# Performance work log

Hardware: AMD Instinct MI355X
Metric: run time of the kernel (lower is better)

Reference implementation:

```python
import jax, jax.numpy as jnp
import numpy as np

EPS = 1e-7
MAX_NORM = 1.0 - 1e-5  # projection radius of the unit Poincare ball (c=1)


def _artanh(x):
    x = jnp.clip(x, -1.0 + 1e-7, 1.0 - 1e-7)
    return 0.5 * (jnp.log1p(x) - jnp.log1p(-x))


def _proj(x):
    # project back onto the open unit ball for numerical stability
    norm = jnp.maximum(jnp.linalg.norm(x, axis=-1, keepdims=True), EPS)
    return jnp.where(norm > MAX_NORM, x / norm * MAX_NORM, x)


def _mobius_add(x, y):
    # x (+) y on the Poincare ball, c = 1
    x2 = jnp.sum(x * x, axis=-1, keepdims=True)
    y2 = jnp.sum(y * y, axis=-1, keepdims=True)
    xy = jnp.sum(x * y, axis=-1, keepdims=True)
    num = (1.0 + 2.0 * xy + y2) * x + (1.0 - x2) * y
    den = 1.0 + 2.0 * xy + x2 * y2
    return num / jnp.maximum(den, EPS)


def _mobius_matvec(x, W):
    # M (x) x = tanh(||Mx||/||x|| * artanh(||x||)) * Mx/||Mx||
    x_norm = jnp.maximum(jnp.linalg.norm(x, axis=-1, keepdims=True), EPS)  # [N,1]
    mx = x @ W.T                                                           # [N,out]
    mx_norm = jnp.maximum(jnp.linalg.norm(mx, axis=-1, keepdims=True), EPS)
    res = jnp.tanh(mx_norm / x_norm * _artanh(x_norm)) * (mx / mx_norm)
    return _proj(res)


def _parallel_transport0(x, v):
    # transport tangent v from origin to x: (lambda_0 / lambda_x) v = (1 - ||x||^2) v
    x2 = jnp.sum(x * x, axis=-1, keepdims=True)
    return (1.0 - x2) * v


def _expmap(x, v):
    # exp_x(v) = x (+) tanh(lambda_x ||v|| / 2) * v / ||v||
    v_norm = jnp.maximum(jnp.linalg.norm(v, axis=-1, keepdims=True), EPS)
    x2 = jnp.sum(x * x, axis=-1, keepdims=True)
    lam = 2.0 / jnp.maximum(1.0 - x2, EPS)
    second = jnp.tanh(0.5 * lam * v_norm) * (v / v_norm)
    return _proj(_mobius_add(x, second))


def setup_inputs() -> dict:
    key = jax.random.key(0)
    kx, kw, kb = jax.random.split(key, 3)
    N, IN, OUT = 262144, 256, 256
    # points strictly inside the unit ball (norm ~ 0.16)
    x = 0.01 * jax.random.normal(kx, (N, IN), dtype=jnp.float32)
    # kaiming_uniform_(a=sqrt(5)) => U(-1/sqrt(fan_in), 1/sqrt(fan_in))
    bound = 1.0 / np.sqrt(IN)
    W = jax.random.uniform(kw, (OUT, IN), dtype=jnp.float32, minval=-bound, maxval=bound)
    b = jax.random.uniform(kb, (OUT,), dtype=jnp.float32, minval=-0.001, maxval=0.001)
    return {"x": x, "W": W, "b": b}


def reference(x, W, b):
    res = _mobius_matvec(x, W)                 # hyperbolic linear transform
    pt = _parallel_transport0(res, b)          # transport bias from origin to res
    return _expmap(res, pt)                    # exponential map at res
```

## Files before the change

kernel.cpp:

```cpp
#include <hip/hip_runtime.h>

#define EPS 1e-7f
#define MAX_NORM (1.0f - 1e-5f)

typedef __attribute__((ext_vector_type(8))) short bf16x8;
typedef __attribute__((ext_vector_type(4))) short short4v;
typedef __attribute__((ext_vector_type(4))) float f32x4;

__device__ __forceinline__ short f2bf(float f){
  unsigned u = __builtin_bit_cast(unsigned, f);
  u = (u + 0x7fffu + ((u >> 16) & 1u)) >> 16;
  return (short)u;
}
__device__ __forceinline__ float bf2f(short s){
  unsigned u = ((unsigned)(unsigned short)s) << 16;
  return __builtin_bit_cast(float, u);
}

__global__ void setup_s_kernel(const float* __restrict__ b, float* __restrict__ s_buf){
  __shared__ float redv[256];
  int t = threadIdx.x;
  float v = b[t];
  redv[t] = v * v;
  __syncthreads();
  for (int off = 128; off > 0; off >>= 1){
    if (t < off) redv[t] += redv[t + off];
    __syncthreads();
  }
  float bn = sqrtf(redv[0]);
  float th = tanhf(bn);
  s_buf[t] = th * v / fmaxf(bn, EPS);
  if (t == 0) s_buf[256] = th * th;
}

__global__ void conv_w_kernel(const float* __restrict__ W, short* __restrict__ WB){
  int idx = blockIdx.x * 256 + threadIdx.x;
  int n = idx >> 8, k = idx & 255;
  int ks = k >> 5, q = (k >> 3) & 3, j = k & 7;
  int dst = ((((n >> 4) * 8 + ks) * 4 + q) * 16 + (n & 15)) * 8 + j;
  WB[dst] = f2bf(W[idx]);
}

__global__ void hyp_main(const float* __restrict__ x, const short* __restrict__ WB,
                         const float* __restrict__ s_buf, float* __restrict__ out){
  __shared__ __align__(16) short A_lds[64 * 264];
  __shared__ float xpart[256];
  __shared__ float redp[4][64][2];
  __shared__ float pq[64][2];

  const int tid = threadIdx.x;
  const int wave = tid >> 6, lane = tid & 63;
  const int quad = lane >> 4, l15 = lane & 15;
  const int m0 = blockIdx.x * 64;

  const float4* xt = (const float4*)(x + (size_t)m0 * 256);
  #pragma unroll
  for (int i = 0; i < 16; i++){
    int f = i * 256 + tid;
    int row = f >> 6, c4 = f & 63;
    float4 v = xt[f];
    short4v p;
    p.x = f2bf(v.x); p.y = f2bf(v.y); p.z = f2bf(v.z); p.w = f2bf(v.w);
    *(short4v*)&A_lds[row * 264 + c4 * 4] = p;
  }
  __syncthreads();

  {
    int row = tid >> 2, seg = tid & 3;
    float sum = 0.f;
    #pragma unroll
    for (int i = 0; i < 8; i++){
      bf16x8 v = *(const bf16x8*)&A_lds[row * 264 + seg * 64 + i * 8];
      #pragma unroll
      for (int j = 0; j < 8; j++){ float f = bf2f(v[j]); sum += f * f; }
    }
    xpart[tid] = sum;
  }

  f32x4 acc[4][4];
  #pragma unroll
  for (int mt = 0; mt < 4; mt++)
    #pragma unroll
    for (int tn = 0; tn < 4; tn++) acc[mt][tn] = (f32x4){0.f, 0.f, 0.f, 0.f};

  const bf16x8* WBv = (const bf16x8*)WB;
  #pragma unroll
  for (int ks = 0; ks < 8; ks++){
    bf16x8 bfrag[4], afrag[4];
    #pragma unroll
    for (int tn = 0; tn < 4; tn++) bfrag[tn] = WBv[((wave * 4 + tn) * 8 + ks) * 64 + lane];
    #pragma unroll
    for (int mt = 0; mt < 4; mt++)
      afrag[mt] = *(const bf16x8*)&A_lds[(mt * 16 + l15) * 264 + ks * 32 + quad * 8];
    #pragma unroll
    for (int mt = 0; mt < 4; mt++)
      #pragma unroll
      for (int tn = 0; tn < 4; tn++)
        acc[mt][tn] = __builtin_amdgcn_mfma_f32_16x16x32_bf16(afrag[mt], bfrag[tn], acc[mt][tn], 0, 0, 0);
  }

  float sv[4];
  #pragma unroll
  for (int tn = 0; tn < 4; tn++) sv[tn] = s_buf[wave * 64 + tn * 16 + l15];

  float msq[4][4], mds[4][4];
  #pragma unroll
  for (int mt = 0; mt < 4; mt++)
    #pragma unroll
    for (int r = 0; r < 4; r++){
      float a = 0.f, d = 0.f;
      #pragma unroll
      for (int tn = 0; tn < 4; tn++){ float c = acc[mt][tn][r]; a += c * c; d += c * sv[tn]; }
      msq[mt][r] = a; mds[mt][r] = d;
    }
  #pragma unroll
  for (int m = 1; m < 16; m <<= 1){
    #pragma unroll
    for (int mt = 0; mt < 4; mt++)
      #pragma unroll
      for (int r = 0; r < 4; r++){
        msq[mt][r] += __shfl_xor(msq[mt][r], m, 64);
        mds[mt][r] += __shfl_xor(mds[mt][r], m, 64);
      }
  }
  if (l15 == 0){
    #pragma unroll
    for (int mt = 0; mt < 4; mt++)
      #pragma unroll
      for (int r = 0; r < 4; r++){
        int row = mt * 16 + quad * 4 + r;
        redp[wave][row][0] = msq[mt][r];
        redp[wave][row][1] = mds[mt][r];
      }
  }
  __syncthreads();

  if (tid < 64){
    int row = tid;
    float ms  = redp[0][row][0] + redp[1][row][0] + redp[2][row][0] + redp[3][row][0];
    float md  = redp[0][row][1] + redp[1][row][1] + redp[2][row][1] + redp[3][row][1];
    float xn2 = xpart[row*4+0] + xpart[row*4+1] + xpart[row*4+2] + xpart[row*4+3];
    float s2 = s_buf[256];
    float xn = fmaxf(sqrtf(xn2), EPS);
    float xc = fminf(xn, 1.0f - 1e-7f);
    float art = 0.5f * (log1pf(xc) - log1pf(-xc));
    float mxn = fmaxf(sqrtf(ms), EPS);
    float tt = tanhf(mxn / xn * art);
    float te = fminf(tt, MAX_NORM);
    float sr = te / mxn;
    float r2 = te * te;
    float xy = sr * md;
    float aa = 1.0f + 2.0f * xy + s2;
    float bc = 1.0f - r2;
    float den = fmaxf(1.0f + 2.0f * xy + r2 * s2, EPS);
    float P = aa * sr / den, Q = bc / den;
    float num2 = aa * aa * r2 + 2.0f * aa * bc * xy + bc * bc * s2;
    float on = fmaxf(sqrtf(num2) / den, EPS);
    if (on > MAX_NORM){ float fsc = MAX_NORM / on; P *= fsc; Q *= fsc; }
    pq[row][0] = P; pq[row][1] = Q;
  }
  __syncthreads();

  float* orow = out + (size_t)m0 * 256;
  #pragma unroll
  for (int mt = 0; mt < 4; mt++)
    #pragma unroll
    for (int r = 0; r < 4; r++){
      int row = mt * 16 + quad * 4 + r;
      float P = pq[row][0], Q = pq[row][1];
      #pragma unroll
      for (int tn = 0; tn < 4; tn++)
        orow[(size_t)row * 256 + wave * 64 + tn * 16 + l15] = P * acc[mt][tn][r] + Q * sv[tn];
    }
}

extern "C" void kernel_launch(void* const* d_in, const int* in_sizes, int n_in,
                              void* d_out, int out_size, void* d_ws, size_t ws_size,
                              hipStream_t stream){
  const float* x = (const float*)d_in[0];
  const float* W = (const float*)d_in[1];
  const float* b = (const float*)d_in[2];
  float* out = (float*)d_out;

  short* WB    = (short*)d_ws;
  float* s_buf = (float*)((char*)d_ws + 256 * 256 * 2);

  int N = in_sizes[0] / 256;

  setup_s_kernel<<<1, 256, 0, stream>>>(b, s_buf);
  conv_w_kernel<<<256, 256, 0, stream>>>(W, WB);
  hyp_main<<<N / 64, 256, 0, stream>>>(x, WB, s_buf, out);
}
```

Before: 478.1 us.

## Compute transposed MFMA per wave on its own rows, dropping LDS and block syncs

Each wave now owns 16 rows and loads x straight from global memory into registers as the MFMA B operand, computing W·x^T so that each lane holds four consecutive output columns of one row. Row norms and the dot product with the bias are reduced with two cross-quad shuffles instead of an LDS staging buffer and two block barriers, and output is written as float4 stores. The x norm is now taken in fp32 before bf16 rounding. In exchange every wave streams the full 256x256 bf16 W from global/L2 rather than a quarter of it, and register pressure rises (16 accumulators plus 8 x fragments), with launch bounds asking for 4 blocks per CU.

```diff
diff --git a/kernel.cpp b/kernel.cpp
--- a/kernel.cpp
+++ b/kernel.cpp
@@ -4,17 +4,12 @@
 #define MAX_NORM (1.0f - 1e-5f)
 
 typedef __attribute__((ext_vector_type(8))) short bf16x8;
-typedef __attribute__((ext_vector_type(4))) short short4v;
 typedef __attribute__((ext_vector_type(4))) float f32x4;
 
 __device__ __forceinline__ short f2bf(float f){
   unsigned u = __builtin_bit_cast(unsigned, f);
   u = (u + 0x7fffu + ((u >> 16) & 1u)) >> 16;
   return (short)u;
-}
-__device__ __forceinline__ float bf2f(short s){
-  unsigned u = ((unsigned)(unsigned short)s) << 16;
-  return __builtin_bit_cast(float, u);
 }
 
 __global__ void setup_s_kernel(const float* __restrict__ b, float* __restrict__ s_buf){
@@ -41,137 +36,95 @@
   WB[dst] = f2bf(W[idx]);
 }
 
-__global__ void hyp_main(const float* __restrict__ x, const short* __restrict__ WB,
-                         const float* __restrict__ s_buf, float* __restrict__ out){
-  __shared__ __align__(16) short A_lds[64 * 264];
-  __shared__ float xpart[256];
-  __shared__ float redp[4][64][2];
-  __shared__ float pq[64][2];
-
+__global__ __launch_bounds__(256, 4)
+void hyp_main(const float* __restrict__ x, const short* __restrict__ WB,
+              const float* __restrict__ s_buf, float* __restrict__ out){
   const int tid = threadIdx.x;
   const int wave = tid >> 6, lane = tid & 63;
   const int quad = lane >> 4, l15 = lane & 15;
-  const int m0 = blockIdx.x * 64;
+  const int row = blockIdx.x * 64 + wave * 16 + l15;
 
-  const float4* xt = (const float4*)(x + (size_t)m0 * 256);
+  const float* xrow = x + (size_t)row * 256;
+  float4 va[8], vb[8];
   #pragma unroll
-  for (int i = 0; i < 16; i++){
-    int f = i * 256 + tid;
-    int row = f >> 6, c4 = f & 63;
-    float4 v = xt[f];
-    short4v p;
-    p.x = f2bf(v.x); p.y = f2bf(v.y); p.z = f2bf(v.z); p.w = f2bf(v.w);
-    *(short4v*)&A_lds[row * 264 + c4 * 4] = p;
-  }
-  __syncthreads();
-
-  {
-    int row = tid >> 2, seg = tid & 3;
-    float sum = 0.f;
-    #pragma unroll
-    for (int i = 0; i < 8; i++){
-      bf16x8 v = *(const bf16x8*)&A_lds[row * 264 + seg * 64 + i * 8];
-      #pragma unroll
-      for (int j = 0; j < 8; j++){ float f = bf2f(v[j]); sum += f * f; }
-    }
-    xpart[tid] = sum;
+  for (int ks = 0; ks < 8; ks++){
+    const float4* p = (const float4*)(xrow + ks * 32 + quad * 8);
+    va[ks] = p[0];
+    vb[ks] = p[1];
   }
 
-  f32x4 acc[4][4];
+  float xn2 = 0.f;
+  bf16x8 xf[8];
   #pragma unroll
-  for (int mt = 0; mt < 4; mt++)
-    #pragma unroll
-    for (int tn = 0; tn < 4; tn++) acc[mt][tn] = (f32x4){0.f, 0.f, 0.f, 0.f};
+  for (int ks = 0; ks < 8; ks++){
+    float f0 = va[ks].x, f1 = va[ks].y, f2 = va[ks].z, f3 = va[ks].w;
+    float f4 = vb[ks].x, f5 = vb[ks].y, f6 = vb[ks].z, f7 = vb[ks].w;
+    xn2 += f0*f0 + f1*f1 + f2*f2 + f3*f3 + f4*f4 + f5*f5 + f6*f6 + f7*f7;
+    bf16x8 p;
+    p[0]=f2bf(f0); p[1]=f2bf(f1); p[2]=f2bf(f2); p[3]=f2bf(f3);
+    p[4]=f2bf(f4); p[5]=f2bf(f5); p[6]=f2bf(f6); p[7]=f2bf(f7);
+    xf[ks] = p;
+  }
+  xn2 += __shfl_xor(xn2, 16, 64);
+  xn2 += __shfl_xor(xn2, 32, 64);
 
   const bf16x8* WBv = (const bf16x8*)WB;
+  f32x4 acc[16];
   #pragma unroll
-  for (int ks = 0; ks < 8; ks++){
-    bf16x8 bfrag[4], afrag[4];
+  for (int tn = 0; tn < 16; tn++){
+    bf16x8 wf[8];
     #pragma unroll
-    for (int tn = 0; tn < 4; tn++) bfrag[tn] = WBv[((wave * 4 + tn) * 8 + ks) * 64 + lane];
+    for (int ks = 0; ks < 8; ks++)
+      wf[ks] = WBv[(tn * 8 + ks) * 64 + lane];
+    f32x4 a = (f32x4){0.f, 0.f, 0.f, 0.f};
     #pragma unroll
-    for (int mt = 0; mt < 4; mt++)
-      afrag[mt] = *(const bf16x8*)&A_lds[(mt * 16 + l15) * 264 + ks * 32 + quad * 8];
-    #pragma unroll
-    for (int mt = 0; mt < 4; mt++)
-      #pragma unroll
-      for (int tn = 0; tn < 4; tn++)
-        acc[mt][tn] = __builtin_amdgcn_mfma_f32_16x16x32_bf16(afrag[mt], bfrag[tn], acc[mt][tn], 0, 0, 0);
+    for (int ks = 0; ks < 8; ks++)
+      a = __builtin_amdgcn_mfma_f32_16x16x32_bf16(wf[ks], xf[ks], a, 0, 0, 0);
+    acc[tn] = a;
   }
 
-  float sv[4];
+  float msq = 0.f, mds = 0.f;
   #pragma unroll
-  for (int tn = 0; tn < 4; tn++) sv[tn] = s_buf[wave * 64 + tn * 16 + l15];
+  for (int tn = 0; tn < 16; tn++){
+    float4 sv4 = *(const float4*)&s_buf[tn * 16 + quad * 4];
+    msq += acc[tn][0]*acc[tn][0] + acc[tn][1]*acc[tn][1]
+         + acc[tn][2]*acc[tn][2] + acc[tn][3]*acc[tn][3];
+    mds += acc[tn][0]*sv4.x + acc[tn][1]*sv4.y + acc[tn][2]*sv4.z + acc[tn][3]*sv4.w;
+  }
+  msq += __shfl_xor(msq, 16, 64);
+  msq += __shfl_xor(msq, 32, 64);
+  mds += __shfl_xor(mds, 16, 64);
+  mds += __shfl_xor(mds, 32, 64);
 
-  float msq[4][4], mds[4][4];
+  float s2 = s_buf[256];
+  float xn = fmaxf(sqrtf(xn2), EPS);
+  float xc = fminf(xn, 1.0f - 1e-7f);
+  float art = 0.5f * (log1pf(xc) - log1pf(-xc));
+  float mxn = fmaxf(sqrtf(msq), EPS);
+  float tt = tanhf(mxn / xn * art);
+  float te = fminf(tt, MAX_NORM);
+  float sr = te / mxn;
+  float r2 = te * te;
+  float xy = sr * mds;
+  float aa = 1.0f + 2.0f * xy + s2;
+  float bc = 1.0f - r2;
+  float den = fmaxf(1.0f + 2.0f * xy + r2 * s2, EPS);
+  float P = aa * sr / den, Q = bc / den;
+  float num2 = aa * aa * r2 + 2.0f * aa * bc * xy + bc * bc * s2;
+  float on = fmaxf(sqrtf(num2) / den, EPS);
+  if (on > MAX_NORM){ float fsc = MAX_NORM / on; P *= fsc; Q *= fsc; }
+
+  float* orow = out + (size_t)row * 256;
   #pragma unroll
-  for (int mt = 0; mt < 4; mt++)
-    #pragma unroll
-    for (int r = 0; r < 4; r++){
-      float a = 0.f, d = 0.f;
-      #pragma unroll
-      for (int tn = 0; tn < 4; tn++){ float c = acc[mt][tn][r]; a += c * c; d += c * sv[tn]; }
-      msq[mt][r] = a; mds[mt][r] = d;
-    }
-  #pragma unroll
-  for (int m = 1; m < 16; m <<= 1){
-    #pragma unroll
-    for (int mt = 0; mt < 4; mt++)
-      #pragma unroll
-      for (int r = 0; r < 4; r++){
-        msq[mt][r] += __shfl_xor(msq[mt][r], m, 64);
-        mds[mt][r] += __shfl_xor(mds[mt][r], m, 64);
-      }
+  for (int tn = 0; tn < 16; tn++){
+    float4 sv4 = *(const float4*)&s_buf[tn * 16 + quad * 4];
+    float4 o;
+    o.x = P * acc[tn][0] + Q * sv4.x;
+    o.y = P * acc[tn][1] + Q * sv4.y;
+    o.z = P * acc[tn][2] + Q * sv4.z;
+    o.w = P * acc[tn][3] + Q * sv4.w;
+    *(float4*)&orow[tn * 16 + quad * 4] = o;
   }
-  if (l15 == 0){
-    #pragma unroll
-    for (int mt = 0; mt < 4; mt++)
-      #pragma unroll
-      for (int r = 0; r < 4; r++){
-        int row = mt * 16 + quad * 4 + r;
-        redp[wave][row][0] = msq[mt][r];
-        redp[wave][row][1] = mds[mt][r];
-      }
-  }
-  __syncthreads();
-
-  if (tid < 64){
-    int row = tid;
-    float ms  = redp[0][row][0] + redp[1][row][0] + redp[2][row][0] + redp[3][row][0];
-    float md  = redp[0][row][1] + redp[1][row][1] + redp[2][row][1] + redp[3][row][1];
-    float xn2 = xpart[row*4+0] + xpart[row*4+1] + xpart[row*4+2] + xpart[row*4+3];
-    float s2 = s_buf[256];
-    float xn = fmaxf(sqrtf(xn2), EPS);
-    float xc = fminf(xn, 1.0f - 1e-7f);
-    float art = 0.5f * (log1pf(xc) - log1pf(-xc));
-    float mxn = fmaxf(sqrtf(ms), EPS);
-    float tt = tanhf(mxn / xn * art);
-    float te = fminf(tt, MAX_NORM);
-    float sr = te / mxn;
-    float r2 = te * te;
-    float xy = sr * md;
-    float aa = 1.0f + 2.0f * xy + s2;
-    float bc = 1.0f - r2;
-    float den = fmaxf(1.0f + 2.0f * xy + r2 * s2, EPS);
-    float P = aa * sr / den, Q = bc / den;
-    float num2 = aa * aa * r2 + 2.0f * aa * bc * xy + bc * bc * s2;
-    float on = fmaxf(sqrtf(num2) / den, EPS);
-    if (on > MAX_NORM){ float fsc = MAX_NORM / on; P *= fsc; Q *= fsc; }
-    pq[row][0] = P; pq[row][1] = Q;
-  }
-  __syncthreads();
-
-  float* orow = out + (size_t)m0 * 256;
-  #pragma unroll
-  for (int mt = 0; mt < 4; mt++)
-    #pragma unroll
-    for (int r = 0; r < 4; r++){
-      int row = mt * 16 + quad * 4 + r;
-      float P = pq[row][0], Q = pq[row][1];
-      #pragma unroll
-      for (int tn = 0; tn < 4; tn++)
-        orow[(size_t)row * 256 + wave * 64 + tn * 16 + l15] = P * acc[mt][tn][r] + Q * sv[tn];
-    }
 }
 
 extern "C" void kernel_launch(void* const* d_in, const int* in_sizes, int n_in,
```

New measurement: 538.3 us. 1.13x slower.
